# Kernel tuning notes

Measured on AMD Instinct MI355X. Metric: run time of the kernel, lower is better.

The kernel has to match this reference:

```python
import jax, jax.numpy as jnp
import numpy as np

HEADS = 8
DIM_HEAD = 32
DIM = HEADS * DIM_HEAD  # 256
B, H, W = 2, 256, 256


def _dw2d(x, wgt):
    # depthwise 3x3 conv, NCHW, weight (C,1,3,3)
    return jax.lax.conv_general_dilated(
        x, wgt, window_strides=(1, 1), padding='SAME',
        feature_group_count=x.shape[1],
        dimension_numbers=('NCHW', 'OIHW', 'NCHW'))


def setup_inputs() -> dict:
    key = jax.random.key(0)
    ks = jax.random.split(key, 20)
    def kaiming(k, shape, fan_in):
        return jax.random.normal(k, shape, jnp.float32) * np.sqrt(2.0 / fan_in)
    inp = {}
    inp['x_in'] = jax.random.normal(ks[0], (B, H, W, DIM), jnp.float32)
    # shared depthwise weights (heads,1,3,3), kaiming_normal fan_in=9
    names = ['qw1', 'qw2', 'qw3', 'kw1', 'kw2', 'kw3', 'vw1', 'vw2', 'vw3']
    for i, n in enumerate(names):
        inp[n] = kaiming(ks[1 + i], (HEADS, 1, 3, 3), 9)
    # pos_emb: two depthwise convs dim->dim with bias
    inp['pos_w1'] = kaiming(ks[10], (DIM, 1, 3, 3), 9)
    inp['pos_b1'] = jnp.zeros((DIM,), jnp.float32)
    inp['pos_w2'] = kaiming(ks[11], (DIM, 1, 3, 3), 9)
    inp['pos_b2'] = jnp.zeros((DIM,), jnp.float32)
    # conv1d heads->heads kernel 3
    inp['conv1d_w'] = kaiming(ks[12], (HEADS, HEADS, 3), HEADS * 3)
    inp['conv1d_b'] = jnp.zeros((HEADS,), jnp.float32)
    inp['rescale'] = jnp.ones((HEADS, 1, 1), jnp.float32)
    inp['rescale2'] = jnp.ones((HEADS, 1, 1), jnp.float32)
    inp['proj_w'] = kaiming(ks[13], (DIM, DIM), DIM)  # (out,in) torch layout
    inp['proj_b'] = jnp.zeros((DIM,), jnp.float32)
    return inp


def reference(x_in, qw1, qw2, qw3, kw1, kw2, kw3, vw1, vw2, vw3,
              pos_w1, pos_b1, pos_w2, pos_b2, conv1d_w, conv1d_b,
              rescale, rescale2, proj_w, proj_b):
    b, h, w, c = x_in.shape
    heads = rescale.shape[0]
    dim_head = c // heads
    x = jnp.transpose(x_in, (0, 3, 1, 2))  # NCHW
    # positional embedding: dwconv -> gelu(exact) -> dwconv
    t = _dw2d(x, pos_w1) + pos_b1[None, :, None, None]
    t = jax.nn.gelu(t, approximate=False)
    t = _dw2d(t, pos_w2) + pos_b2[None, :, None, None]
    x = x + t

    def chain(x, w1, w2, w3):
        for wgt in (w1, w2, w3):
            x = _dw2d(x, jnp.repeat(wgt, dim_head, axis=0))
        return x

    q = chain(x, qw1, qw2, qw3)
    k = chain(x, kw1, kw2, kw3)
    v = chain(x, vw1, vw2, vw3)
    # (b,c,h,w) -> (b,heads,dim_head,hw) ; channel = head*dim_head + d
    q = q.reshape(b, heads, dim_head, h * w)
    k = k.reshape(b, heads, dim_head, h * w)
    v = v.reshape(b, heads, dim_head, h * w)
    eps = 1e-12
    q = q / jnp.maximum(jnp.linalg.norm(q, axis=-1, keepdims=True), eps)
    k = k / jnp.maximum(jnp.linalg.norm(k, axis=-1, keepdims=True), eps)
    # channel attention: k @ q^T -> (b,heads,dim_head,dim_head)
    attn = jnp.einsum('bhdn,bhen->bhde', k, q)
    # pooled v -> conv1d over dim_head length, channels = heads
    y = v.mean(axis=-1)  # (b,heads,dim_head)
    attn_v = jax.lax.conv_general_dilated(
        y, conv1d_w, window_strides=(1,), padding='SAME',
        dimension_numbers=('NCH', 'OIH', 'NCH')) + conv1d_b[None, :, None]
    diag = attn_v[..., :, None] * jnp.eye(dim_head, dtype=attn.dtype)
    attn = attn * rescale[None] + diag * rescale2[None]
    attn = jax.nn.softmax(attn, axis=-1)
    out = jnp.einsum('bhde,bhen->bhdn', attn, v)  # (b,heads,dim_head,hw)
    out = jnp.transpose(out, (0, 3, 1, 2)).reshape(b, h * w, c)
    out = out @ proj_w.T + proj_b
    return out.reshape(b, h, w, c)
```

## Files before the change

kernel.cpp:

```cpp
#include <hip/hip_runtime.h>
#include <stdint.h>
#include <math.h>


using u16 = unsigned short;
using u32 = unsigned int;

typedef __bf16 bf16x8_t __attribute__((ext_vector_type(8)));
typedef float f32x4_t __attribute__((ext_vector_type(4)));

__device__ __forceinline__ float bf2f(u16 v) {
  u32 u = ((u32)v) << 16;
  return __builtin_bit_cast(float, u);
}
__device__ __forceinline__ u16 f2bf(float f) {
  u32 u = __builtin_bit_cast(u32, f);
  u32 r = u + 0x7fffu + ((u >> 16) & 1u);
  return (u16)(r >> 16);
}
__device__ __forceinline__ void unpack8(uint4 u, float f[8]) {
  f[0] = bf2f((u16)(u.x & 0xffffu)); f[1] = bf2f((u16)(u.x >> 16));
  f[2] = bf2f((u16)(u.y & 0xffffu)); f[3] = bf2f((u16)(u.y >> 16));
  f[4] = bf2f((u16)(u.z & 0xffffu)); f[5] = bf2f((u16)(u.z >> 16));
  f[6] = bf2f((u16)(u.w & 0xffffu)); f[7] = bf2f((u16)(u.w >> 16));
}
__device__ __forceinline__ uint4 pack8(const u16 o[8]) {
  uint4 v;
  v.x = (u32)o[0] | ((u32)o[1] << 16);
  v.y = (u32)o[2] | ((u32)o[3] << 16);
  v.z = (u32)o[4] | ((u32)o[5] << 16);
  v.w = (u32)o[6] | ((u32)o[7] << 16);
  return v;
}
__device__ __forceinline__ uint2 pack4(const u16 o[4]) {
  uint2 v;
  v.x = (u32)o[0] | ((u32)o[1] << 16);
  v.y = (u32)o[2] | ((u32)o[3] << 16);
  return v;
}

__global__ __launch_bounds__(256) void compose_kernel(
    const float* __restrict__ qw1, const float* __restrict__ qw2,
    const float* __restrict__ qw3, const float* __restrict__ kw1,
    const float* __restrict__ kw2, const float* __restrict__ kw3,
    const float* __restrict__ vw1, const float* __restrict__ vw2,
    const float* __restrict__ vw3, u16* __restrict__ Tab) {
  __shared__ float Wf[24][49];
  const int t = threadIdx.x;
  if (t < 24) {
    const int h = t / 3, c = t % 3;
    const float* w1 = (c == 0 ? qw1 : c == 1 ? kw1 : vw1) + h * 9;
    const float* w2 = (c == 0 ? qw2 : c == 1 ? kw2 : vw2) + h * 9;
    const float* w3 = (c == 0 ? qw3 : c == 1 ? kw3 : vw3) + h * 9;
    float w12[25];
    for (int i = 0; i < 25; ++i) w12[i] = 0.f;
    for (int ky = 0; ky < 3; ++ky)
      for (int kx = 0; kx < 3; ++kx)
        for (int ly = 0; ly < 3; ++ly)
          for (int lx = 0; lx < 3; ++lx)
            w12[(ky + ly) * 5 + kx + lx] += w2[ky * 3 + kx] * w1[ly * 3 + lx];
    float we[49];
    for (int i = 0; i < 49; ++i) we[i] = 0.f;
    for (int my = 0; my < 3; ++my)
      for (int mx = 0; mx < 3; ++mx)
        for (int ey = 0; ey < 5; ++ey)
          for (int ex = 0; ex < 5; ++ex)
            we[(my + ey) * 7 + mx + ex] += w3[my * 3 + mx] * w12[ey * 5 + ex];
    for (int i = 0; i < 49; ++i) Wf[t][i] = we[i];
  }
  __syncthreads();
  for (int e = t; e < 21504; e += 256) {
    const int lane = e & 63;
    int r1 = e >> 6;
    const int dy = r1 % 7;
    int r2 = r1 / 7;
    const int part = r2 & 1;
    const int hc = r2 >> 1;
    const int x = lane & 15, q = lane >> 4;
    u16 ov[8];
#pragma unroll
    for (int j = 0; j < 8; ++j) {
      const int d = q * 8 + j - x;
      const float wv = (d >= 0 && d < 7) ? Wf[hc][dy * 7 + d] : 0.f;
      const u16 hb = f2bf(wv);
      ov[j] = (part == 0) ? hb : f2bf(wv - bf2f(hb));
    }
    *reinterpret_cast<uint4*>(Tab + (size_t)e * 8) = pack8(ov);
  }
}

__global__ __launch_bounds__(256) void posemb_kernel(
    const float* __restrict__ xin, u16* __restrict__ x2,
    const float* __restrict__ w1g, const float* __restrict__ b1g,
    const float* __restrict__ w2g, const float* __restrict__ b2g) {
  const int t = threadIdx.x;
  const int o = t & 3;
  const int bz = blockIdx.z;
  const int cg = bz & 7;
  const int b = bz >> 3;
  const int x0 = blockIdx.x * 16;
  const int y0 = blockIdx.y * 8;
  const int c0 = cg * 32 + o * 8;

  __shared__ __align__(16) u16 Abuf[240 * 32];
  __shared__ __align__(16) u16 Bbuf[180 * 32];

  for (int i = t; i < 240 * 4; i += 256) {
    const int px = i >> 2, oo = i & 3;
    const int lx = px % 20, ly = px / 20;
    const int gx = x0 - 2 + lx, gy = y0 - 2 + ly;
    u16 ov[8];
    if (gx >= 0 && gx < 256 && gy >= 0 && gy < 256) {
      const float* p = xin + ((size_t)((b << 16) + (gy << 8) + gx)) * 256 + cg * 32 + oo * 8;
      const float4 r0 = *reinterpret_cast<const float4*>(p);
      const float4 r1 = *reinterpret_cast<const float4*>(p + 4);
      ov[0] = f2bf(r0.x); ov[1] = f2bf(r0.y); ov[2] = f2bf(r0.z); ov[3] = f2bf(r0.w);
      ov[4] = f2bf(r1.x); ov[5] = f2bf(r1.y); ov[6] = f2bf(r1.z); ov[7] = f2bf(r1.w);
    } else {
#pragma unroll
      for (int j = 0; j < 8; ++j) ov[j] = 0;
    }
    *reinterpret_cast<uint4*>(Abuf + px * 32 + oo * 8) = pack8(ov);
  }
  __syncthreads();

  {
    float w[72], bi[8];
#pragma unroll
    for (int j = 0; j < 8; ++j) {
#pragma unroll
      for (int k = 0; k < 9; ++k) w[j * 9 + k] = w1g[(c0 + j) * 9 + k];
      bi[j] = b1g[c0 + j];
    }
    for (int i = t; i < 180 * 4; i += 256) {
      const int px = i >> 2;
      const int sx = px % 18, sy = px / 18;
      const int gx = x0 - 1 + sx, gy = y0 - 1 + sy;
      const bool inb = (gx >= 0 && gx < 256 && gy >= 0 && gy < 256);
      float a[8];
#pragma unroll
      for (int j = 0; j < 8; ++j) a[j] = bi[j];
#pragma unroll
      for (int ky = 0; ky < 3; ++ky)
#pragma unroll
        for (int kx = 0; kx < 3; ++kx) {
          float f[8];
          unpack8(*reinterpret_cast<const uint4*>(
                      Abuf + ((sy + ky) * 20 + sx + kx) * 32 + o * 8), f);
#pragma unroll
          for (int j = 0; j < 8; ++j) a[j] = fmaf(w[j * 9 + ky * 3 + kx], f[j], a[j]);
        }
      u16 ov[8];
#pragma unroll
      for (int j = 0; j < 8; ++j) {
        const float g = 0.5f * a[j] * (1.0f + erff(a[j] * 0.70710678118654752f));
        ov[j] = inb ? f2bf(g) : (u16)0;
      }
      *reinterpret_cast<uint4*>(Bbuf + px * 32 + o * 8) = pack8(ov);
    }
  }
  __syncthreads();

  {
    float w[72], bi[8];
#pragma unroll
    for (int j = 0; j < 8; ++j) {
#pragma unroll
      for (int k = 0; k < 9; ++k) w[j * 9 + k] = w2g[(c0 + j) * 9 + k];
      bi[j] = b2g[c0 + j];
    }
    for (int i = t; i < 128 * 4; i += 256) {
      const int px = i >> 2;
      const int sx = px & 15, sy = px >> 4;
      float a[8];
#pragma unroll
      for (int j = 0; j < 8; ++j) a[j] = bi[j];
#pragma unroll
      for (int ky = 0; ky < 3; ++ky)
#pragma unroll
        for (int kx = 0; kx < 3; ++kx) {
          float f[8];
          unpack8(*reinterpret_cast<const uint4*>(
                      Bbuf + ((sy + ky) * 18 + sx + kx) * 32 + o * 8), f);
#pragma unroll
          for (int j = 0; j < 8; ++j) a[j] = fmaf(w[j * 9 + ky * 3 + kx], f[j], a[j]);
        }
      float xr[8];
      unpack8(*reinterpret_cast<const uint4*>(
                  Abuf + ((sy + 2) * 20 + sx + 2) * 32 + o * 8), xr);
      u16 ov[8];
#pragma unroll
      for (int j = 0; j < 8; ++j) ov[j] = f2bf(a[j] + xr[j]);
      u16* dst = x2 + ((size_t)((b << 16) + ((y0 + sy) << 8) + x0 + sx)) * 256 + cg * 32 + o * 8;
      *reinterpret_cast<uint4*>(dst) = pack8(ov);
    }
  }
}

__global__ __launch_bounds__(256) void qkv_fused_kernel(
    const u16* __restrict__ x2, u16* __restrict__ v3out,
    const u16* __restrict__ Tab, float* __restrict__ G,
    float* __restrict__ sqq, float* __restrict__ sqk,
    float* __restrict__ vsum) {
  const int t = threadIdx.x;
  const int wave = t >> 6;
  const int lane = t & 63;
  const int q = lane >> 4;
  const int n = lane & 15;
  const int choff = n >> 3;
  const int yy = n & 7;
  const int bz = blockIdx.z;
  const int h = bz & 7;
  const int b = bz >> 3;
  const int x0 = (blockIdx.x + 1) * 16;
  const int y0 = (blockIdx.y + 1) * 8;

  __shared__ __align__(16) u16 Xt[10768];

  u32* XtW = reinterpret_cast<u32*>(Xt);
  for (int i = t; i < 520; i += 256) {
    if (i < 512) {
      const int ch = i >> 4, row = i & 15;
      if (row < 14) XtW[ch * 168 + row * 12 + 11] = 0u;
    } else {
      XtW[5376 + (i - 512)] = 0u;
    }
  }

  for (int px = lane; px < 308; px += 64) {
    const int ly = px / 22, lx = px - ly * 22;
    const int gx = x0 - 3 + lx, gy = y0 - 3 + ly;
    const uint4 v = *reinterpret_cast<const uint4*>(
        x2 + ((size_t)((b << 16) + (gy << 8) + gx)) * 256 + h * 32 + wave * 8);
    u16* dst = Xt + (wave * 8) * 336 + ly * 24 + lx;
    dst[0]    = (u16)(v.x & 0xffffu); dst[336]  = (u16)(v.x >> 16);
    dst[672]  = (u16)(v.y & 0xffffu); dst[1008] = (u16)(v.y >> 16);
    dst[1344] = (u16)(v.z & 0xffffu); dst[1680] = (u16)(v.z >> 16);
    dst[2016] = (u16)(v.w & 0xffffu); dst[2352] = (u16)(v.w >> 16);
  }
  __syncthreads();

  f32x4_t acc[3][4];
#pragma unroll
  for (int c = 0; c < 3; ++c)
#pragma unroll
    for (int pl = 0; pl < 4; ++pl) acc[c][pl] = {0.f, 0.f, 0.f, 0.f};

  const u16* TabL = Tab + (size_t)h * 21504 + (size_t)lane * 8;
  int rowb[4];
#pragma unroll
  for (int pl = 0; pl < 4; ++pl)
    rowb[pl] = (2 * (wave * 4 + pl) + choff) * 336 + yy * 24 + q * 8;

#pragma unroll
  for (int dy = 0; dy < 7; ++dy) {
    bf16x8_t Ah[3], Al[3];
#pragma unroll
    for (int c = 0; c < 3; ++c) {
      Ah[c] = *reinterpret_cast<const bf16x8_t*>(TabL + (size_t)((c * 2 + 0) * 7 + dy) * 512);
      Al[c] = *reinterpret_cast<const bf16x8_t*>(TabL + (size_t)((c * 2 + 1) * 7 + dy) * 512);
    }
#pragma unroll
    for (int pl = 0; pl < 4; ++pl) {
      const bf16x8_t Bv = *reinterpret_cast<const bf16x8_t*>(&Xt[rowb[pl] + dy * 24]);
      acc[0][pl] = __builtin_amdgcn_mfma_f32_16x16x32_bf16(Ah[0], Bv, acc[0][pl], 0, 0, 0);
      acc[1][pl] = __builtin_amdgcn_mfma_f32_16x16x32_bf16(Ah[1], Bv, acc[1][pl], 0, 0, 0);
      acc[2][pl] = __builtin_amdgcn_mfma_f32_16x16x32_bf16(Ah[2], Bv, acc[2][pl], 0, 0, 0);
      acc[0][pl] = __builtin_amdgcn_mfma_f32_16x16x32_bf16(Al[0], Bv, acc[0][pl], 0, 0, 0);
      acc[1][pl] = __builtin_amdgcn_mfma_f32_16x16x32_bf16(Al[1], Bv, acc[1][pl], 0, 0, 0);
      acc[2][pl] = __builtin_amdgcn_mfma_f32_16x16x32_bf16(Al[2], Bv, acc[2][pl], 0, 0, 0);
    }
  }
  __syncthreads();

  u16* K3s = Xt;
  u16* Q3s = Xt + 32 * 132;

  const int masks[5] = {1, 2, 4, 16, 32};
#pragma unroll
  for (int pl = 0; pl < 4; ++pl) {
    const int ch = 2 * (wave * 4 + pl) + choff;
    float sq = 0.f, sk = 0.f, sv = 0.f;
    u16 qb[4], kb[4], vb[4];
#pragma unroll
    for (int r = 0; r < 4; ++r) {
      qb[r] = f2bf(acc[0][pl][r]);
      const float qf = bf2f(qb[r]); sq = fmaf(qf, qf, sq);
      kb[r] = f2bf(acc[1][pl][r]);
      const float kf = bf2f(kb[r]); sk = fmaf(kf, kf, sk);
      vb[r] = f2bf(acc[2][pl][r]);
      sv += bf2f(vb[r]);
    }
    *reinterpret_cast<uint2*>(&Q3s[ch * 132 + yy * 16 + q * 4]) = pack4(qb);
    *reinterpret_cast<uint2*>(&K3s[ch * 132 + yy * 16 + q * 4]) = pack4(kb);
    u16* vp = v3out + ((size_t)((b << 16) + ((y0 + yy) << 8) + (x0 + q * 4))) * 256 + h * 32 + ch;
    vp[0] = vb[0]; vp[256] = vb[1]; vp[512] = vb[2]; vp[768] = vb[3];
#pragma unroll
    for (int mi = 0; mi < 5; ++mi) {
      sq += __shfl_xor(sq, masks[mi]);
      sk += __shfl_xor(sk, masks[mi]);
      sv += __shfl_xor(sv, masks[mi]);
    }
    if ((lane & 55) == 0) {
      atomicAdd(&sqq[b * 256 + h * 32 + ch], sq);
      atomicAdd(&sqk[b * 256 + h * 32 + ch], sk);
      atomicAdd(&vsum[b * 256 + h * 32 + ch], sv);
    }
  }
  __syncthreads();

  const int d0 = (wave & 1) * 16;
  const int e0 = (wave >> 1) * 16;
  f32x4_t ga = {0.f, 0.f, 0.f, 0.f};
#pragma unroll
  for (int kb4 = 0; kb4 < 4; ++kb4) {
    const bf16x8_t avf = *reinterpret_cast<const bf16x8_t*>(
        &K3s[(d0 + n) * 132 + kb4 * 32 + q * 8]);
    const bf16x8_t bvf = *reinterpret_cast<const bf16x8_t*>(
        &Q3s[(e0 + n) * 132 + kb4 * 32 + q * 8]);
    ga = __builtin_amdgcn_mfma_f32_16x16x32_bf16(avf, bvf, ga, 0, 0, 0);
  }
  float* Gp = G + (size_t)((b * 8 + h) * 32) * 32;
#pragma unroll
  for (int r = 0; r < 4; ++r)
    atomicAdd(&Gp[(d0 + q * 4 + r) * 32 + e0 + n], ga[r]);
}

__device__ __forceinline__ void border_map(int bi, int& bx, int& by) {
  if (bi < 16) { bx = bi; by = 0; }
  else if (bi < 32) { bx = bi - 16; by = 31; }
  else { const int e = bi - 32; by = 1 + (e >> 1); bx = (e & 1) * 15; }
}

template <int RED, int BORDER>
__global__ __launch_bounds__(256) void chain3_kernel(
    const u16* __restrict__ in, u16* __restrict__ out,
    const float* __restrict__ w1g, const float* __restrict__ w2g,
    const float* __restrict__ w3g, float* __restrict__ red) {
  const int t = threadIdx.x;
  const int o = t & 3;
  const int bz = blockIdx.z;
  const int h = bz & 7;
  const int b = bz >> 3;
  int bx = blockIdx.x, by = blockIdx.y;
  if (BORDER) border_map(blockIdx.x, bx, by);
  const int x0 = bx * 16;
  const int y0 = by * 8;

  __shared__ __align__(16) u16 Abuf[308 * 32];
  __shared__ __align__(16) u16 Bbuf[240 * 32];
  __shared__ float rbuf[32];
  if (t < 32) rbuf[t] = 0.f;

  float w1[9], w2[9], w3[9];
#pragma unroll
  for (int k = 0; k < 9; ++k) {
    w1[k] = w1g[h * 9 + k];
    w2[k] = w2g[h * 9 + k];
    w3[k] = w3g[h * 9 + k];
  }

  for (int i = t; i < 308 * 4; i += 256) {
    const int px = i >> 2, oo = i & 3;
    const int lx = px % 22, ly = px / 22;
    const int gx = x0 - 3 + lx, gy = y0 - 3 + ly;
    uint4 v = {0, 0, 0, 0};
    if (gx >= 0 && gx < 256 && gy >= 0 && gy < 256)
      v = *reinterpret_cast<const uint4*>(
          in + ((size_t)((b << 16) + (gy << 8) + gx)) * 256 + h * 32 + oo * 8);
    *reinterpret_cast<uint4*>(Abuf + px * 32 + oo * 8) = v;
  }
  __syncthreads();

  for (int i = t; i < 240 * 4; i += 256) {
    const int px = i >> 2;
    const int sx = px % 20, sy = px / 20;
    const int gx = x0 - 2 + sx, gy = y0 - 2 + sy;
    const bool inb = (gx >= 0 && gx < 256 && gy >= 0 && gy < 256);
    float a[8] = {0, 0, 0, 0, 0, 0, 0, 0};
#pragma unroll
    for (int ky = 0; ky < 3; ++ky)
#pragma unroll
      for (int kx = 0; kx < 3; ++kx) {
        float f[8];
        unpack8(*reinterpret_cast<const uint4*>(
                    Abuf + ((sy + ky) * 22 + sx + kx) * 32 + o * 8), f);
#pragma unroll
        for (int j = 0; j < 8; ++j) a[j] = fmaf(w1[ky * 3 + kx], f[j], a[j]);
      }
    u16 ov[8];
#pragma unroll
    for (int j = 0; j < 8; ++j) ov[j] = inb ? f2bf(a[j]) : (u16)0;
    *reinterpret_cast<uint4*>(Bbuf + px * 32 + o * 8) = pack8(ov);
  }
  __syncthreads();

  for (int i = t; i < 180 * 4; i += 256) {
    const int px = i >> 2;
    const int sx = px % 18, sy = px / 18;
    const int gx = x0 - 1 + sx, gy = y0 - 1 + sy;
    const bool inb = (gx >= 0 && gx < 256 && gy >= 0 && gy < 256);
    float a[8] = {0, 0, 0, 0, 0, 0, 0, 0};
#pragma unroll
    for (int ky = 0; ky < 3; ++ky)
#pragma unroll
      for (int kx = 0; kx < 3; ++kx) {
        float f[8];
        unpack8(*reinterpret_cast<const uint4*>(
                    Bbuf + ((sy + ky) * 20 + sx + kx) * 32 + o * 8), f);
#pragma unroll
        for (int j = 0; j < 8; ++j) a[j] = fmaf(w2[ky * 3 + kx], f[j], a[j]);
      }
    u16 ov[8];
#pragma unroll
    for (int j = 0; j < 8; ++j) ov[j] = inb ? f2bf(a[j]) : (u16)0;
    *reinterpret_cast<uint4*>(Abuf + px * 32 + o * 8) = pack8(ov);
  }
  __syncthreads();

  float racc[8] = {0, 0, 0, 0, 0, 0, 0, 0};
  for (int i = t; i < 128 * 4; i += 256) {
    const int px = i >> 2;
    const int sx = px & 15, sy = px >> 4;
    float a[8] = {0, 0, 0, 0, 0, 0, 0, 0};
#pragma unroll
    for (int ky = 0; ky < 3; ++ky)
#pragma unroll
      for (int kx = 0; kx < 3; ++kx) {
        float f[8];
        unpack8(*reinterpret_cast<const uint4*>(
                    Abuf + ((sy + ky) * 18 + sx + kx) * 32 + o * 8), f);
#pragma unroll
        for (int j = 0; j < 8; ++j) a[j] = fmaf(w3[ky * 3 + kx], f[j], a[j]);
      }
    u16 ov[8];
#pragma unroll
    for (int j = 0; j < 8; ++j) {
      ov[j] = f2bf(a[j]);
      const float rv = bf2f(ov[j]);
      if (RED == 1) racc[j] = fmaf(rv, rv, racc[j]);
      if (RED == 2) racc[j] += rv;
    }
    u16* dst = out + ((size_t)((b << 16) + ((y0 + sy) << 8) + x0 + sx)) * 256 + h * 32 + o * 8;
    *reinterpret_cast<uint4*>(dst) = pack8(ov);
  }
  __syncthreads();
#pragma unroll
  for (int j = 0; j < 8; ++j) atomicAdd(&rbuf[o * 8 + j], racc[j]);
  __syncthreads();
  if (t < 32) atomicAdd(&red[b * 256 + h * 32 + t], rbuf[t]);
}

template <int BORDER>
__global__ __launch_bounds__(256) void kchain_gram_kernel(
    const u16* __restrict__ in, const u16* __restrict__ q3,
    const float* __restrict__ w1g, const float* __restrict__ w2g,
    const float* __restrict__ w3g, float* __restrict__ G, float* __restrict__ sqk) {
  const int t = threadIdx.x;
  const int o = t & 3;
  const int bz = blockIdx.z;
  const int h = bz & 7;
  const int b = bz >> 3;
  int bx = blockIdx.x, by = blockIdx.y;
  if (BORDER) border_map(blockIdx.x, bx, by);
  const int x0 = bx * 16;
  const int y0 = by * 8;

  __shared__ __align__(16) u16 Abuf[308 * 32];
  __shared__ __align__(16) u16 Bbuf[240 * 32];
  __shared__ __align__(16) u16 K3s[32 * 132];
  __shared__ __align__(16) u16 Q3s[32 * 132];
  __shared__ float rbuf[32];
  if (t < 32) rbuf[t] = 0.f;

  float w1[9], w2[9], w3[9];
#pragma unroll
  for (int k = 0; k < 9; ++k) {
    w1[k] = w1g[h * 9 + k];
    w2[k] = w2g[h * 9 + k];
    w3[k] = w3g[h * 9 + k];
  }

  for (int i = t; i < 308 * 4; i += 256) {
    const int px = i >> 2, oo = i & 3;
    const int lx = px % 22, ly = px / 22;
    const int gx = x0 - 3 + lx, gy = y0 - 3 + ly;
    uint4 v = {0, 0, 0, 0};
    if (gx >= 0 && gx < 256 && gy >= 0 && gy < 256)
      v = *reinterpret_cast<const uint4*>(
          in + ((size_t)((b << 16) + (gy << 8) + gx)) * 256 + h * 32 + oo * 8);
    *reinterpret_cast<uint4*>(Abuf + px * 32 + oo * 8) = v;
  }
  __syncthreads();

  for (int i = t; i < 240 * 4; i += 256) {
    const int px = i >> 2;
    const int sx = px % 20, sy = px / 20;
    const int gx = x0 - 2 + sx, gy = y0 - 2 + sy;
    const bool inb = (gx >= 0 && gx < 256 && gy >= 0 && gy < 256);
    float a[8] = {0, 0, 0, 0, 0, 0, 0, 0};
#pragma unroll
    for (int ky = 0; ky < 3; ++ky)
#pragma unroll
      for (int kx = 0; kx < 3; ++kx) {
        float f[8];
        unpack8(*reinterpret_cast<const uint4*>(
                    Abuf + ((sy + ky) * 22 + sx + kx) * 32 + o * 8), f);
#pragma unroll
        for (int j = 0; j < 8; ++j) a[j] = fmaf(w1[ky * 3 + kx], f[j], a[j]);
      }
    u16 ov[8];
#pragma unroll
    for (int j = 0; j < 8; ++j) ov[j] = inb ? f2bf(a[j]) : (u16)0;
    *reinterpret_cast<uint4*>(Bbuf + px * 32 + o * 8) = pack8(ov);
  }
  __syncthreads();

  for (int i = t; i < 180 * 4; i += 256) {
    const int px = i >> 2;
    const int sx = px % 18, sy = px / 18;
    const int gx = x0 - 1 + sx, gy = y0 - 1 + sy;
    const bool inb = (gx >= 0 && gx < 256 && gy >= 0 && gy < 256);
    float a[8] = {0, 0, 0, 0, 0, 0, 0, 0};
#pragma unroll
    for (int ky = 0; ky < 3; ++ky)
#pragma unroll
      for (int kx = 0; kx < 3; ++kx) {
        float f[8];
        unpack8(*reinterpret_cast<const uint4*>(
                    Bbuf + ((sy + ky) * 20 + sx + kx) * 32 + o * 8), f);
#pragma unroll
        for (int j = 0; j < 8; ++j) a[j] = fmaf(w2[ky * 3 + kx], f[j], a[j]);
      }
    u16 ov[8];
#pragma unroll
    for (int j = 0; j < 8; ++j) ov[j] = inb ? f2bf(a[j]) : (u16)0;
    *reinterpret_cast<uint4*>(Abuf + px * 32 + o * 8) = pack8(ov);
  }
  __syncthreads();

  float racc[8] = {0, 0, 0, 0, 0, 0, 0, 0};
  for (int i = t; i < 128 * 4; i += 256) {
    const int px = i >> 2;
    const int sx = px & 15, sy = px >> 4;
    float a[8] = {0, 0, 0, 0, 0, 0, 0, 0};
#pragma unroll
    for (int ky = 0; ky < 3; ++ky)
#pragma unroll
      for (int kx = 0; kx < 3; ++kx) {
        float f[8];
        unpack8(*reinterpret_cast<const uint4*>(
                    Abuf + ((sy + ky) * 18 + sx + kx) * 32 + o * 8), f);
#pragma unroll
        for (int j = 0; j < 8; ++j) a[j] = fmaf(w3[ky * 3 + kx], f[j], a[j]);
      }
#pragma unroll
    for (int j = 0; j < 8; ++j) {
      const u16 kb16 = f2bf(a[j]);
      const float kv = bf2f(kb16);
      K3s[(o * 8 + j) * 132 + px] = kb16;
      racc[j] = fmaf(kv, kv, racc[j]);
    }
    const uint4 uq = *reinterpret_cast<const uint4*>(
        q3 + ((size_t)((b << 16) + ((y0 + sy) << 8) + x0 + sx)) * 256 + h * 32 + o * 8);
    Q3s[(o * 8 + 0) * 132 + px] = (u16)(uq.x & 0xffffu);
    Q3s[(o * 8 + 1) * 132 + px] = (u16)(uq.x >> 16);
    Q3s[(o * 8 + 2) * 132 + px] = (u16)(uq.y & 0xffffu);
    Q3s[(o * 8 + 3) * 132 + px] = (u16)(uq.y >> 16);
    Q3s[(o * 8 + 4) * 132 + px] = (u16)(uq.z & 0xffffu);
    Q3s[(o * 8 + 5) * 132 + px] = (u16)(uq.z >> 16);
    Q3s[(o * 8 + 6) * 132 + px] = (u16)(uq.w & 0xffffu);
    Q3s[(o * 8 + 7) * 132 + px] = (u16)(uq.w >> 16);
  }
  __syncthreads();
#pragma unroll
  for (int j = 0; j < 8; ++j) atomicAdd(&rbuf[o * 8 + j], racc[j]);
  __syncthreads();
  if (t < 32) atomicAdd(&sqk[b * 256 + h * 32 + t], rbuf[t]);

  const int wave = t >> 6;
  const int lane = t & 63;
  const int quad = lane >> 4;
  const int l15 = lane & 15;
  const int d0 = (wave & 1) * 16;
  const int e0 = (wave >> 1) * 16;
  f32x4_t acc = {0.f, 0.f, 0.f, 0.f};
#pragma unroll
  for (int kb = 0; kb < 4; ++kb) {
    const bf16x8_t av = *reinterpret_cast<const bf16x8_t*>(
        &K3s[(d0 + l15) * 132 + kb * 32 + quad * 8]);
    const bf16x8_t bv = *reinterpret_cast<const bf16x8_t*>(
        &Q3s[(e0 + l15) * 132 + kb * 32 + quad * 8]);
    acc = __builtin_amdgcn_mfma_f32_16x16x32_bf16(av, bv, acc, 0, 0, 0);
  }
  float* Gp = G + (size_t)((b * 8 + h) * 32) * 32;
#pragma unroll
  for (int r = 0; r < 4; ++r)
    atomicAdd(&Gp[(d0 + quad * 4 + r) * 32 + e0 + l15], acc[r]);
}

__global__ __launch_bounds__(256) void attn_kernel(
    const float* __restrict__ G, const float* __restrict__ sqq,
    const float* __restrict__ sqk, const float* __restrict__ vsum,
    const float* __restrict__ cw, const float* __restrict__ cb,
    const float* __restrict__ rs1, const float* __restrict__ rs2,
    float* __restrict__ attn) {
  const int b = blockIdx.x;
  const int t = threadIdx.x;
  const int h = t >> 5;
  const int d = t & 31;
  __shared__ float vm[8][34];
  __shared__ float nq[256];
  vm[h][d + 1] = vsum[b * 256 + t] * (1.0f / 65536.0f);
  if (t < 8) { vm[t][0] = 0.f; vm[t][33] = 0.f; }
  nq[t] = fmaxf(sqrtf(sqq[b * 256 + t]), 1e-12f);
  __syncthreads();

  float av = cb[h];
#pragma unroll
  for (int i = 0; i < 8; ++i)
#pragma unroll
    for (int tau = 0; tau < 3; ++tau)
      av = fmaf(cw[h * 24 + i * 3 + tau], vm[i][d + tau], av);

  const float nk = fmaxf(sqrtf(sqk[b * 256 + t]), 1e-12f);
  const float rsc = rs1[h];
  const float rsc2 = rs2[h];
  const float* Gp = G + (size_t)((b * 8 + h) * 32 + d) * 32;
  float L[32];
#pragma unroll
  for (int e = 0; e < 32; ++e) {
    float l = Gp[e] * rsc / (nk * nq[h * 32 + e]);
    if (e == d) l += av * rsc2;
    L[e] = l;
  }
  float mx = L[0];
#pragma unroll
  for (int e = 1; e < 32; ++e) mx = fmaxf(mx, L[e]);
  float s = 0.f;
#pragma unroll
  for (int e = 0; e < 32; ++e) {
    L[e] = expf(L[e] - mx);
    s += L[e];
  }
  const float inv = 1.0f / s;
  float* Ap = attn + (size_t)((b * 8 + h) * 32 + d) * 32;
#pragma unroll
  for (int e = 0; e < 32; ++e) Ap[e] = L[e] * inv;
}

__global__ __launch_bounds__(256) void mbuild_kernel(
    const float* __restrict__ attn, const float* __restrict__ pw,
    u16* __restrict__ M) {
  const int bid = blockIdx.x;
  const int b = bid >> 3;
  const int h = bid & 7;
  const int t = threadIdx.x;
  __shared__ float at[32][33];
#pragma unroll
  for (int i = 0; i < 4; ++i) {
    const int idx = t * 4 + i;
    at[idx >> 5][idx & 31] = attn[(size_t)(b * 8 + h) * 1024 + idx];
  }
  __syncthreads();
  float pwf[32];
#pragma unroll
  for (int dd = 0; dd < 32; ++dd) pwf[dd] = pw[(size_t)t * 256 + h * 32 + dd];
  u16* Mp = M + (size_t)b * 65536 + (size_t)t * 256 + h * 32;
#pragma unroll
  for (int e = 0; e < 32; ++e) {
    float s = 0.f;
#pragma unroll
    for (int dd = 0; dd < 32; ++dd) s = fmaf(pwf[dd], at[dd][e], s);
    Mp[e] = f2bf(s);
  }
}

__global__ __launch_bounds__(256) void gemm_kernel(
    const u16* __restrict__ V, const u16* __restrict__ Mm,
    const float* __restrict__ pb, float* __restrict__ out) {
  const int m0 = blockIdx.x * 128;
  const int n0 = blockIdx.y * 64;
  const int b = m0 >> 16;
  const u16* Mb = Mm + (size_t)b * 65536;

  __shared__ __align__(16) u16 As[128][72];
  __shared__ __align__(16) u16 Bs[64][72];

  const int t = threadIdx.x;
  const int wave = t >> 6;
  const int lane = t & 63;
  const int quad = lane >> 4;
  const int l15 = lane & 15;

  f32x4_t acc[2][4];
#pragma unroll
  for (int mt = 0; mt < 2; ++mt)
#pragma unroll
    for (int nt = 0; nt < 4; ++nt) acc[mt][nt] = {0.f, 0.f, 0.f, 0.f};

  for (int k0 = 0; k0 < 256; k0 += 64) {
#pragma unroll
    for (int i = 0; i < 4; ++i) {
      const int id = t + 256 * i;
      const int row = id >> 3;
      const int c8 = id & 7;
      *reinterpret_cast<uint4*>(&As[row][c8 * 8]) = *reinterpret_cast<const uint4*>(
          &V[(size_t)(m0 + row) * 256 + k0 + c8 * 8]);
    }
#pragma unroll
    for (int i = 0; i < 2; ++i) {
      const int id = t + 256 * i;
      const int row = id >> 3;
      const int c8 = id & 7;
      *reinterpret_cast<uint4*>(&Bs[row][c8 * 8]) = *reinterpret_cast<const uint4*>(
          &Mb[(size_t)(n0 + row) * 256 + k0 + c8 * 8]);
    }
    __syncthreads();
#pragma unroll
    for (int ks = 0; ks < 2; ++ks) {
      bf16x8_t af[2], bfv[4];
#pragma unroll
      for (int mt = 0; mt < 2; ++mt)
        af[mt] = *reinterpret_cast<const bf16x8_t*>(
            &As[wave * 32 + mt * 16 + l15][ks * 32 + quad * 8]);
#pragma unroll
      for (int nt = 0; nt < 4; ++nt)
        bfv[nt] = *reinterpret_cast<const bf16x8_t*>(
            &Bs[nt * 16 + l15][ks * 32 + quad * 8]);
#pragma unroll
      for (int mt = 0; mt < 2; ++mt)
#pragma unroll
        for (int nt = 0; nt < 4; ++nt)
          acc[mt][nt] =
              __builtin_amdgcn_mfma_f32_16x16x32_bf16(af[mt], bfv[nt], acc[mt][nt], 0, 0, 0);
    }
    __syncthreads();
  }

#pragma unroll
  for (int nt = 0; nt < 4; ++nt) {
    const int col = n0 + nt * 16 + l15;
    const float pbf = pb[col];
#pragma unroll
    for (int mt = 0; mt < 2; ++mt) {
#pragma unroll
      for (int r = 0; r < 4; ++r) {
        const int m = m0 + wave * 32 + mt * 16 + quad * 4 + r;
        out[(size_t)m * 256 + col] = acc[mt][nt][r] + pbf;
      }
    }
  }
}

extern "C" void kernel_launch(void* const* d_in, const int* in_sizes, int n_in,
                              void* d_out, int out_size, void* d_ws, size_t ws_size,
                              hipStream_t stream) {
  const float* x_in = (const float*)d_in[0];
  const float* qw1 = (const float*)d_in[1];
  const float* qw2 = (const float*)d_in[2];
  const float* qw3 = (const float*)d_in[3];
  const float* kw1 = (const float*)d_in[4];
  const float* kw2 = (const float*)d_in[5];
  const float* kw3 = (const float*)d_in[6];
  const float* vw1 = (const float*)d_in[7];
  const float* vw2 = (const float*)d_in[8];
  const float* vw3 = (const float*)d_in[9];
  const float* posw1 = (const float*)d_in[10];
  const float* posb1 = (const float*)d_in[11];
  const float* posw2 = (const float*)d_in[12];
  const float* posb2 = (const float*)d_in[13];
  const float* cw = (const float*)d_in[14];
  const float* cb = (const float*)d_in[15];
  const float* rs1 = (const float*)d_in[16];
  const float* rs2 = (const float*)d_in[17];
  const float* pw = (const float*)d_in[18];
  const float* pb = (const float*)d_in[19];

  char* ws = (char*)d_ws;
  const size_t SLOT = 67108864;
  u16* S0 = (u16*)(ws);
  u16* S1 = (u16*)(ws + SLOT);
  u16* D0 = (u16*)d_out;
  char* SM = ws + 2 * SLOT;
  float* G = (float*)(SM);
  float* sqq = (float*)(SM + 65536);
  float* sqk = (float*)(SM + 67584);
  float* vsum = (float*)(SM + 69632);
  float* attn = (float*)(SM + 71680);
  u16* Mm = (u16*)(SM + 137216);
  u16* Tab = (u16*)((char*)d_out + 100663296);

  hipMemsetAsync(SM, 0, 71680, stream);

  compose_kernel<<<1, 256, 0, stream>>>(qw1, qw2, qw3, kw1, kw2, kw3,
                                        vw1, vw2, vw3, Tab);

  const dim3 tgrid(16, 32, 16);
  posemb_kernel<<<tgrid, 256, 0, stream>>>(x_in, S0, posw1, posb1, posw2, posb2);

  qkv_fused_kernel<<<dim3(14, 30, 16), 256, 0, stream>>>(S0, S1, Tab, G, sqq, sqk, vsum);

  const dim3 bgrid(92, 1, 16);
  chain3_kernel<1, 1><<<bgrid, 256, 0, stream>>>(S0, D0, qw1, qw2, qw3, sqq);
  kchain_gram_kernel<1><<<bgrid, 256, 0, stream>>>(S0, D0, kw1, kw2, kw3, G, sqk);
  chain3_kernel<2, 1><<<bgrid, 256, 0, stream>>>(S0, S1, vw1, vw2, vw3, vsum);

  attn_kernel<<<2, 256, 0, stream>>>(G, sqq, sqk, vsum, cw, cb, rs1, rs2, attn);
  mbuild_kernel<<<16, 256, 0, stream>>>(attn, pw, Mm);
  gemm_kernel<<<dim3(1024, 4), 256, 0, stream>>>(S1, Mm, pb, (float*)d_out);
}
```

Before: 1.027 ms.

## Stage V output through LDS for coalesced stores and prefetch MFMA weights

Three changes to the qkv kernel. V results are staged in shared memory and written out as 16-byte vectorized pixel-contiguous stores, replacing scattered 2-byte global stores. The weight table loads for the next dy are issued ahead of the current MFMA batch (register double buffering). A min-blocks-per-CU hint of 3 is added. The larger LDS footprint and the extra registers can reduce occupancy, and the register cap from the launch bound may cause spills.

```diff
diff --git a/kernel.cpp b/kernel.cpp
--- a/kernel.cpp
+++ b/kernel.cpp
@@ -197,7 +197,7 @@
   }
 }
 
-__global__ __launch_bounds__(256) void qkv_fused_kernel(
+__global__ __launch_bounds__(256, 3) void qkv_fused_kernel(
     const u16* __restrict__ x2, u16* __restrict__ v3out,
     const u16* __restrict__ Tab, float* __restrict__ G,
     float* __restrict__ sqq, float* __restrict__ sqk,
@@ -215,7 +215,8 @@
   const int x0 = (blockIdx.x + 1) * 16;
   const int y0 = (blockIdx.y + 1) * 8;
 
-  __shared__ __align__(16) u16 Xt[10768];
+  __shared__ __align__(16) u16 Sh[13568];
+  u16* Xt = Sh;
 
   u32* XtW = reinterpret_cast<u32*>(Xt);
   for (int i = t; i < 520; i += 256) {
@@ -252,29 +253,36 @@
   for (int pl = 0; pl < 4; ++pl)
     rowb[pl] = (2 * (wave * 4 + pl) + choff) * 336 + yy * 24 + q * 8;
 
+  bf16x8_t Ac[6], An[6];
+#pragma unroll
+  for (int c6 = 0; c6 < 6; ++c6)
+    Ac[c6] = *reinterpret_cast<const bf16x8_t*>(TabL + (size_t)(c6 * 7 + 0) * 512);
+
 #pragma unroll
   for (int dy = 0; dy < 7; ++dy) {
-    bf16x8_t Ah[3], Al[3];
-#pragma unroll
-    for (int c = 0; c < 3; ++c) {
-      Ah[c] = *reinterpret_cast<const bf16x8_t*>(TabL + (size_t)((c * 2 + 0) * 7 + dy) * 512);
-      Al[c] = *reinterpret_cast<const bf16x8_t*>(TabL + (size_t)((c * 2 + 1) * 7 + dy) * 512);
+    if (dy < 6) {
+#pragma unroll
+      for (int c6 = 0; c6 < 6; ++c6)
+        An[c6] = *reinterpret_cast<const bf16x8_t*>(TabL + (size_t)(c6 * 7 + dy + 1) * 512);
     }
 #pragma unroll
     for (int pl = 0; pl < 4; ++pl) {
       const bf16x8_t Bv = *reinterpret_cast<const bf16x8_t*>(&Xt[rowb[pl] + dy * 24]);
-      acc[0][pl] = __builtin_amdgcn_mfma_f32_16x16x32_bf16(Ah[0], Bv, acc[0][pl], 0, 0, 0);
-      acc[1][pl] = __builtin_amdgcn_mfma_f32_16x16x32_bf16(Ah[1], Bv, acc[1][pl], 0, 0, 0);
-      acc[2][pl] = __builtin_amdgcn_mfma_f32_16x16x32_bf16(Ah[2], Bv, acc[2][pl], 0, 0, 0);
-      acc[0][pl] = __builtin_amdgcn_mfma_f32_16x16x32_bf16(Al[0], Bv, acc[0][pl], 0, 0, 0);
-      acc[1][pl] = __builtin_amdgcn_mfma_f32_16x16x32_bf16(Al[1], Bv, acc[1][pl], 0, 0, 0);
-      acc[2][pl] = __builtin_amdgcn_mfma_f32_16x16x32_bf16(Al[2], Bv, acc[2][pl], 0, 0, 0);
-    }
-  }
-  __syncthreads();
-
-  u16* K3s = Xt;
-  u16* Q3s = Xt + 32 * 132;
+#pragma unroll
+      for (int c6 = 0; c6 < 6; ++c6)
+        acc[c6 >> 1][pl] =
+            __builtin_amdgcn_mfma_f32_16x16x32_bf16(Ac[c6], Bv, acc[c6 >> 1][pl], 0, 0, 0);
+    }
+    if (dy < 6) {
+#pragma unroll
+      for (int c6 = 0; c6 < 6; ++c6) Ac[c6] = An[c6];
+    }
+  }
+  __syncthreads();
+
+  u16* K3s = Sh;
+  u16* Q3s = Sh + 4224;
+  u16* V3s = Sh + 8448;
 
   const int masks[5] = {1, 2, 4, 16, 32};
 #pragma unroll
@@ -293,8 +301,8 @@
     }
     *reinterpret_cast<uint2*>(&Q3s[ch * 132 + yy * 16 + q * 4]) = pack4(qb);
     *reinterpret_cast<uint2*>(&K3s[ch * 132 + yy * 16 + q * 4]) = pack4(kb);
-    u16* vp = v3out + ((size_t)((b << 16) + ((y0 + yy) << 8) + (x0 + q * 4))) * 256 + h * 32 + ch;
-    vp[0] = vb[0]; vp[256] = vb[1]; vp[512] = vb[2]; vp[768] = vb[3];
+#pragma unroll
+    for (int r = 0; r < 4; ++r) V3s[(yy * 16 + q * 4 + r) * 40 + ch] = vb[r];
 #pragma unroll
     for (int mi = 0; mi < 5; ++mi) {
       sq += __shfl_xor(sq, masks[mi]);
@@ -308,6 +316,14 @@
     }
   }
   __syncthreads();
+
+  for (int i = t; i < 512; i += 256) {
+    const int px = i >> 2, o = i & 3;
+    const uint4 v = *reinterpret_cast<const uint4*>(&V3s[px * 40 + o * 8]);
+    const int gy = y0 + (px >> 4), gx = x0 + (px & 15);
+    *reinterpret_cast<uint4*>(
+        v3out + ((size_t)((b << 16) + (gy << 8) + gx)) * 256 + h * 32 + o * 8) = v;
+  }
 
   const int d0 = (wave & 1) * 16;
   const int e0 = (wave >> 1) * 16;
```

After: 1.011 ms. No clear change (-1.6%).
